# Kernel tuning notes

Measured on AMD Instinct MI355X. Metric: run time of the kernel, lower is better.

The kernel has to match this reference:

```python
import jax, jax.numpy as jnp
import numpy as np

B, S, DIM = 2, 2048, 2048
H, DN, DR, DV, L = 16, 128, 64, 128, 512  # heads, nope, rope, v, kv_lora_rank
EPS = 1e-5


def setup_inputs() -> dict:
    key = jax.random.key(0)
    ks = jax.random.split(key, 12)
    x = jax.random.normal(ks[0], (B, S, DIM), dtype=jnp.float32)
    # rotary tables (DeepSeek-style: theta = 10000^{-2i/d})
    inv_freq = 1.0 / (10000.0 ** (jnp.arange(0, DR, 2, dtype=jnp.float32) / DR))
    ang = jnp.arange(S, dtype=jnp.float32)[:, None] * inv_freq[None, :]  # [S, DR/2]
    freqs_cos = jnp.cos(ang)
    freqs_sin = jnp.sin(ang)
    w = 0.02
    wq_w = jax.random.normal(ks[1], (H * (DN + DR), DIM), dtype=jnp.float32) * w
    wq_b = jnp.zeros((H * (DN + DR),), dtype=jnp.float32)
    wkv_a_w = jax.random.normal(ks[2], (L + DR, DIM), dtype=jnp.float32) * w
    wkv_a_b = jnp.zeros((L + DR,), dtype=jnp.float32)
    kv_norm_g = jnp.ones((L,), dtype=jnp.float32)
    kv_norm_b = jnp.zeros((L,), dtype=jnp.float32)
    wkv_b_w = jax.random.normal(ks[3], (H * (DN + DV), L), dtype=jnp.float32) * w
    wo_w = jax.random.normal(ks[4], (DIM, H * DV), dtype=jnp.float32) * w
    wo_b = jnp.zeros((DIM,), dtype=jnp.float32)
    return {"x": x, "start_pos": 0, "freqs_cos": freqs_cos, "freqs_sin": freqs_sin,
            "wq_w": wq_w, "wq_b": wq_b, "wkv_a_w": wkv_a_w, "wkv_a_b": wkv_a_b,
            "kv_norm_g": kv_norm_g, "kv_norm_b": kv_norm_b, "wkv_b_w": wkv_b_w,
            "wo_w": wo_w, "wo_b": wo_b}


def _rope(t, cos, sin):
    # t: [B, S, n, DR] interpreted as interleaved (re, im) pairs
    tr = t.reshape(*t.shape[:-1], DR // 2, 2)
    re, im = tr[..., 0], tr[..., 1]
    c = cos[None, :, None, :]
    s = sin[None, :, None, :]
    out = jnp.stack([re * c - im * s, re * s + im * c], axis=-1)
    return out.reshape(t.shape)


def _layernorm(v, g, b):
    mu = jnp.mean(v, axis=-1, keepdims=True)
    var = jnp.mean(jnp.square(v - mu), axis=-1, keepdims=True)
    return (v - mu) * jax.lax.rsqrt(var + EPS) * g + b


def reference(x, start_pos, freqs_cos, freqs_sin, wq_w, wq_b, wkv_a_w, wkv_a_b,
              kv_norm_g, kv_norm_b, wkv_b_w, wo_w, wo_b):
    bsz, seqlen, _ = x.shape
    scale = (DN + DR) ** -0.5
    # q projection
    q = (x @ wq_w.T + wq_b).reshape(bsz, seqlen, H, DN + DR)
    q_nope, q_pe = q[..., :DN], q[..., DN:]
    q_pe = _rope(q_pe, freqs_cos, freqs_sin)
    # kv projection
    kv_full = x @ wkv_a_w.T + wkv_a_b
    kv, k_pe = kv_full[..., :L], kv_full[..., L:]
    k_pe = _rope(k_pe[:, :, None, :], freqs_cos, freqs_sin)[:, :, 0, :]  # [B,S,DR]
    kvn = _layernorm(kv, kv_norm_g, kv_norm_b)  # compressed kv cache entries [B,S,L]
    wkv_b = wkv_b_w.reshape(H, DN + DV, L)
    # absorption: fold wkv_b's k-part into q_nope
    q_abs = jnp.einsum('bshd,hdc->bshc', q_nope, wkv_b[:, :DN])
    scores = (jnp.einsum('bshc,btc->bsht', q_abs, kvn)
              + jnp.einsum('bshr,btr->bsht', q_pe, k_pe)) * scale
    # causal mask (query global pos = start_pos + s, key pos = t)
    qpos = jnp.arange(seqlen) + start_pos
    tpos = jnp.arange(seqlen)
    causal = qpos[:, None] >= tpos[None, :]  # [S, T]
    scores = jnp.where(causal[None, :, None, :], scores, -jnp.inf)
    p = jax.nn.softmax(scores.astype(jnp.float32), axis=-1).astype(x.dtype)
    # compressed attention output then un-absorb v
    ctx = jnp.einsum('bsht,btc->bshc', p, kvn)
    out = jnp.einsum('bshc,hdc->bshd', ctx, wkv_b[:, -DV:])
    return out.reshape(bsz, seqlen, H * DV) @ wo_w.T + wo_b
```

## Files before the change

kernel.cpp:

```cpp
#include <hip/hip_runtime.h>
#include <stdint.h>

typedef __attribute__((ext_vector_type(8))) __bf16 bf16x8;
typedef __attribute__((ext_vector_type(4))) float  f32x4;
typedef __attribute__((ext_vector_type(8))) unsigned short u16x8;
typedef __attribute__((ext_vector_type(2))) unsigned int u32x2;
typedef __attribute__((ext_vector_type(4))) unsigned int u32x4;

typedef __attribute__((address_space(1))) void AS1void;
typedef __attribute__((address_space(3))) void AS3void;
typedef __attribute__((address_space(3))) const unsigned char AS3c;

__device__ __forceinline__ float b2f(unsigned short u) {
  unsigned x = ((unsigned)u) << 16; float f; __builtin_memcpy(&f, &x, 4); return f;
}
__device__ __forceinline__ unsigned short f2b(float f) {
  unsigned x; __builtin_memcpy(&x, &f, 4);
  unsigned r = (x + 0x7fffu + ((x >> 16) & 1u)) >> 16;
  return (unsigned short)r;
}
__device__ __forceinline__ void gload16(const void* g, void* l) {
  __builtin_amdgcn_global_load_lds((AS1void*)(void*)g, (AS3void*)l, 16, 0, 0);
}
__device__ __forceinline__ bf16x8 mk8(u32x2 a, u32x2 b) {
  u32x4 t; t[0] = a[0]; t[1] = a[1]; t[2] = b[0]; t[3] = b[1];
  bf16x8 r; __builtin_memcpy(&r, &t, 16); return r;
}
template<int OFF>
__device__ __forceinline__ u32x2 tr_read(AS3c* vp) {
  u32x2 r;
  asm volatile("ds_read_b64_tr_b16 %0, %1 offset:%2"
               : "=&v"(r) : "v"(vp), "n"(OFF));
  return r;
}

__global__ __launch_bounds__(256) void k_cast(const float* __restrict__ in,
                                              unsigned short* __restrict__ out, long n) {
  long i = ((long)blockIdx.x * 256 + threadIdx.x) * 4;
  if (i >= n) return;
  float4 v = *(const float4*)(in + i);
  ushort4 o;
  o.x = f2b(v.x); o.y = f2b(v.y); o.z = f2b(v.z); o.w = f2b(v.w);
  *(ushort4*)(out + i) = o;
}

__global__ __launch_bounds__(256) void k_prep_wkvb(const float* __restrict__ wkvb,
                                                   unsigned short* __restrict__ kT,
                                                   unsigned short* __restrict__ vv) {
  long i = (long)blockIdx.x * 256 + threadIdx.x;
  {
    int d = (int)(i & 127); long r = i >> 7; int c = (int)(r & 511); int h = (int)(r >> 9);
    kT[i] = f2b(wkvb[((long)(h * 256 + d)) * 512 + c]);
  }
  {
    int c = (int)(i & 511); long r = i >> 9; int d = (int)(r & 127); int h = (int)(r >> 7);
    vv[i] = f2b(wkvb[((long)(h * 256 + 128 + d)) * 512 + c]);
  }
}

template<int OUTF32, int BIAS>
__global__ __launch_bounds__(256, 2) void k_gemm_bt(
    const unsigned short* __restrict__ A, long lda, long aSb, long aSh,
    const unsigned short* __restrict__ B, long ldb, long bSb, long bSh,
    void* __restrict__ Cp, long ldc, long cSb, long cSh,
    const float* __restrict__ bias,
    int M, int N, int K, int zH) {
  __shared__ __align__(16) unsigned short sA[128 * 32];
  __shared__ __align__(16) unsigned short sB[128 * 32];
  const int z = blockIdx.z, zb = z / zH, zh = z % zH;
  const unsigned short* Ab = A + zb * aSb + zh * aSh;
  const unsigned short* Bb = B + zb * bSb + zh * bSh;
  const long cOff = (long)zb * cSb + (long)zh * cSh;
  const int n0 = blockIdx.x * 128, m0 = blockIdx.y * 128;
  const int t = threadIdx.x, w = t >> 6, l = t & 63;
  const int wr = (w >> 1) * 64, wc = (w & 1) * 64;
  const int lr = l & 15, lg = l >> 4;
  f32x4 acc[4][4] = {};
  for (int k0 = 0; k0 < K; k0 += 32) {
    #pragma unroll
    for (int cc = 0; cc < 2; ++cc) {
      int c = t + cc * 256;
      int row = c >> 2, col = (c & 3) * 8;
      int ar = m0 + row; ar = ar < M ? ar : M - 1;
      int br = n0 + row; br = br < N ? br : N - 1;
      gload16(Ab + (long)ar * lda + k0 + col, (char*)sA + c * 16);
      gload16(Bb + (long)br * ldb + k0 + col, (char*)sB + c * 16);
    }
    __syncthreads();
    bf16x8 af[4], bf[4];
    #pragma unroll
    for (int i = 0; i < 4; ++i) af[i] = *(const bf16x8*)&sA[(wr + i * 16 + lr) * 32 + lg * 8];
    #pragma unroll
    for (int j = 0; j < 4; ++j) bf[j] = *(const bf16x8*)&sB[(wc + j * 16 + lr) * 32 + lg * 8];
    #pragma unroll
    for (int i = 0; i < 4; ++i)
      #pragma unroll
      for (int j = 0; j < 4; ++j)
        acc[i][j] = __builtin_amdgcn_mfma_f32_16x16x32_bf16(af[i], bf[j], acc[i][j], 0, 0, 0);
    __syncthreads();
  }
  #pragma unroll
  for (int i = 0; i < 4; ++i) {
    #pragma unroll
    for (int r = 0; r < 4; ++r) {
      int row = m0 + wr + i * 16 + lg * 4 + r;
      if (row >= M) continue;
      #pragma unroll
      for (int j = 0; j < 4; ++j) {
        int col = n0 + wc + j * 16 + lr;
        if (col >= N) continue;
        float v = acc[i][j][r];
        if (BIAS) v += bias[col];
        if (OUTF32) ((float*)Cp)[cOff + (long)row * ldc + col] = v;
        else ((unsigned short*)Cp)[cOff + (long)row * ldc + col] = f2b(v);
      }
    }
  }
}

__global__ __launch_bounds__(256) void k_ln(const unsigned short* __restrict__ kvb,
                                            const float* __restrict__ g,
                                            const float* __restrict__ be,
                                            unsigned short* __restrict__ kcat) {
  const int w = threadIdx.x >> 6, l = threadIdx.x & 63;
  const long row = (long)blockIdx.x * 4 + w;
  const unsigned short* src = kvb + row * 576 + l * 8;
  u16x8 v = *(const u16x8*)src;
  float f[8]; float s = 0.f, s2 = 0.f;
  #pragma unroll
  for (int j = 0; j < 8; ++j) { f[j] = b2f(v[j]); s += f[j]; s2 += f[j] * f[j]; }
  #pragma unroll
  for (int m = 1; m < 64; m <<= 1) { s += __shfl_xor(s, m); s2 += __shfl_xor(s2, m); }
  float mu = s * (1.f / 512.f);
  float var = s2 * (1.f / 512.f) - mu * mu;
  float rs = rsqrtf(var + 1e-5f);
  u16x8 o;
  #pragma unroll
  for (int j = 0; j < 8; ++j) {
    int c = l * 8 + j;
    o[j] = f2b((f[j] - mu) * rs * g[c] + be[c]);
  }
  *(u16x8*)(kcat + row * 576 + l * 8) = o;
}

__global__ __launch_bounds__(256) void k_rope_k(const unsigned short* __restrict__ kvb,
                                                const float* __restrict__ fc,
                                                const float* __restrict__ fs,
                                                unsigned short* __restrict__ kcat) {
  int i = blockIdx.x * 256 + threadIdx.x;
  int p = i & 31; int r = i >> 5;
  int s = r & 2047; int b = r >> 11;
  long base = ((long)(b * 2048 + s)) * 576 + 512 + 2 * p;
  float re = b2f(kvb[base]), im = b2f(kvb[base + 1]);
  float c = fc[s * 32 + p], sn = fs[s * 32 + p];
  kcat[base] = f2b(re * c - im * sn);
  kcat[base + 1] = f2b(re * sn + im * c);
}

__global__ __launch_bounds__(256) void k_rope_q(const unsigned short* __restrict__ qfull,
                                                const float* __restrict__ fc,
                                                const float* __restrict__ fs,
                                                unsigned short* __restrict__ qcat) {
  long i = (long)blockIdx.x * 256 + threadIdx.x;
  int p = (int)(i & 31); long r = i >> 5;
  int h = (int)(r & 15); r >>= 4;
  int s = (int)(r & 2047); int b = (int)(r >> 11);
  const unsigned short* src = qfull + ((long)(b * 2048 + s)) * 3072 + h * 192 + 128 + 2 * p;
  float re = b2f(src[0]), im = b2f(src[1]);
  float c = fc[s * 32 + p], sn = fs[s * 32 + p];
  unsigned short* dst = qcat + ((long)((b * 16 + h) * 2048 + s)) * 576 + 512 + 2 * p;
  dst[0] = f2b(re * c - im * sn);
  dst[1] = f2b(re * sn + im * c);
}

__global__ __launch_bounds__(256, 2) void k_attn(
    const unsigned short* __restrict__ qcat,
    const unsigned short* __restrict__ kcat,
    unsigned short* __restrict__ ctx,
    const int* __restrict__ spp) {
  __shared__ __align__(16) char smem[78336];
  const int id = blockIdx.x;
  const int rr = id & 7;
  const int b = rr >> 2;
  const int local = (id >> 3) * 4 + (rr & 3);
  const int qb = 31 - (local >> 4);
  const int h = local & 15;
  const int t = threadIdx.x, w = t >> 6, l = t & 63;
  const int lq = l & 15, hh = l >> 4;
  const int sp = spp[0];
  const long bh = (long)(b * 16 + h);
  const long qrow0 = bh * 2048 + qb * 64 + w * 16;
  const float scale = 0.07216878364870323f;

  bf16x8 qf[18];
  #pragma unroll
  for (int kk = 0; kk < 18; ++kk)
    qf[kk] = *(const bf16x8*)&qcat[(qrow0 + lq) * 576 + kk * 32 + hh * 8];

  f32x4 acc[8][4];
  #pragma unroll
  for (int i = 0; i < 8; ++i)
    #pragma unroll
    for (int j = 0; j < 4; ++j) acc[i][j] = (f32x4){0.f, 0.f, 0.f, 0.f};
  float mrun = -1e30f, lrun = 0.f;
  const int qg = qb * 64 + w * 16 + lq + sp;
  int tmax = qb * 64 + 63 + sp; if (tmax > 2047) tmax = 2047;

  const unsigned short* kbase = kcat + (long)b * 2048 * 576;

  auto STAGE = [&](int bi, int t0) {
    char* dK = smem + bi * 36864;
    #pragma unroll
    for (int cc = 0; cc < 9; ++cc) {
      int c = t + cc * 256;
      int tt = ((c >> 3) & 7) * 4 + ((c >> 1) & 3);
      int gc = (c >> 6) * 16 + (c & 1) * 8;
      gload16(kbase + (long)(t0 + tt) * 576 + gc, dK + c * 16);
    }
  };

  STAGE(0, 0);
  int cur = 0;
  unsigned short* sP = (unsigned short*)(smem + 73728);
  float* sAl = (float*)(smem + 77824);
  int* sNeed = (int*)(smem + 78080);
  const int qrow = w * 16 + lq;
  const int xq = ((qrow >> 1) & 3) << 4;
  const int vcol = (hh * 16) ^ (((lq >> 1) & 3) << 4);
  const int kq = ((lq >> 2) << 7) + ((lq & 3) << 5) + ((hh & 1) << 4) + ((hh >> 1) << 10);

  for (int t0 = 0; t0 <= tmax; t0 += 32) {
    const bool pref = (t0 + 32 <= tmax);
    if (pref) {
      STAGE(cur ^ 1, t0 + 32);
      asm volatile("s_waitcnt vmcnt(9)" ::: "memory");
    } else {
      asm volatile("s_waitcnt vmcnt(0)" ::: "memory");
    }
    __builtin_amdgcn_sched_barrier(0);
    __builtin_amdgcn_s_barrier();
    __builtin_amdgcn_sched_barrier(0);

    const char* sKc = smem + cur * 36864;
    f32x4 sc[2];
    sc[0] = (f32x4){0.f,0.f,0.f,0.f}; sc[1] = (f32x4){0.f,0.f,0.f,0.f};
    __builtin_amdgcn_s_setprio(1);
    #pragma unroll
    for (int tf = 0; tf < 2; ++tf) {
      const char* rb = sKc + kq + tf * 512;
      #pragma unroll
      for (int kk = 0; kk < 18; ++kk) {
        bf16x8 kf = *(const bf16x8*)(rb + kk * 2048);
        sc[tf] = __builtin_amdgcn_mfma_f32_16x16x32_bf16(kf, qf[kk], sc[tf], 0, 0, 0);
      }
    }
    __builtin_amdgcn_s_setprio(0);

    float v[2][4];
    float mt = -1e30f;
    #pragma unroll
    for (int tf = 0; tf < 2; ++tf)
      #pragma unroll
      for (int r = 0; r < 4; ++r) {
        int tg = t0 + tf * 16 + 4 * hh + r;
        v[tf][r] = (tg <= qg) ? sc[tf][r] * scale : -1e30f;
        mt = fmaxf(mt, v[tf][r]);
      }
    mt = fmaxf(mt, __shfl_xor(mt, 16));
    mt = fmaxf(mt, __shfl_xor(mt, 32));
    float al = 1.f;
    unsigned long long needb = __ballot(mt > mrun + 8.f);
    if (needb) {
      float mn = fmaxf(mrun, mt);
      al = __expf(mrun - mn);
      mrun = mn;
      lrun *= al;
    }
    float sr = 0.f;
    #pragma unroll
    for (int tf = 0; tf < 2; ++tf) {
      ushort4 pk;
      float e0 = __expf(v[tf][0] - mrun);
      float e1 = __expf(v[tf][1] - mrun);
      float e2 = __expf(v[tf][2] - mrun);
      float e3 = __expf(v[tf][3] - mrun);
      sr += (e0 + e1) + (e2 + e3);
      pk.x = f2b(e0); pk.y = f2b(e1); pk.z = f2b(e2); pk.w = f2b(e3);
      *(ushort4*)((char*)sP + qrow * 64 + ((32 * tf + 8 * hh) ^ xq)) = pk;
    }
    sr += __shfl_xor(sr, 16);
    sr += __shfl_xor(sr, 32);
    lrun += sr;
    if (l < 16) sAl[w * 16 + l] = al;
    if (l == 0) sNeed[w] = needb ? 1 : 0;
    asm volatile("s_waitcnt lgkmcnt(0)" ::: "memory");
    __builtin_amdgcn_sched_barrier(0);
    __builtin_amdgcn_s_barrier();
    __builtin_amdgcn_sched_barrier(0);

    int needAny = sNeed[0] | sNeed[1] | sNeed[2] | sNeed[3];
    if (needAny) {
      float a4[4];
      #pragma unroll
      for (int q2 = 0; q2 < 4; ++q2) a4[q2] = sAl[q2 * 16 + lq];
      #pragma unroll
      for (int cb = 0; cb < 8; ++cb)
        #pragma unroll
        for (int q2 = 0; q2 < 4; ++q2) acc[cb][q2] *= a4[q2];
    }
    bf16x8 pf0 = *(const bf16x8*)((char*)sP + (0 * 16 + lq) * 64 + vcol);
    bf16x8 pf1 = *(const bf16x8*)((char*)sP + (1 * 16 + lq) * 64 + vcol);
    bf16x8 pf2 = *(const bf16x8*)((char*)sP + (2 * 16 + lq) * 64 + vcol);
    bf16x8 pf3 = *(const bf16x8*)((char*)sP + (3 * 16 + lq) * 64 + vcol);
    __builtin_amdgcn_sched_barrier(0);
    AS3c* vp3 = (AS3c*)(smem + cur * 36864 + (w * 8192) + hh * 256 + lq * 8);
    u32x2 A0, A1, B0, B1, C0, C1, D0, D1;
    #define TRR2(d0, d1, CB) do { \
      d0 = tr_read<(CB) * 1024>(vp3); \
      d1 = tr_read<(CB) * 1024 + 128>(vp3); } while (0)
    #define PVC(CB, E0, E1) do { \
      bf16x8 vf = mk8(E0, E1); \
      acc[CB][0] = __builtin_amdgcn_mfma_f32_16x16x32_bf16(vf, pf0, acc[CB][0], 0, 0, 0); \
      acc[CB][1] = __builtin_amdgcn_mfma_f32_16x16x32_bf16(vf, pf1, acc[CB][1], 0, 0, 0); \
      acc[CB][2] = __builtin_amdgcn_mfma_f32_16x16x32_bf16(vf, pf2, acc[CB][2], 0, 0, 0); \
      acc[CB][3] = __builtin_amdgcn_mfma_f32_16x16x32_bf16(vf, pf3, acc[CB][3], 0, 0, 0); } while (0)
    TRR2(A0, A1, 0); TRR2(B0, B1, 1);
    TRR2(C0, C1, 2); TRR2(D0, D1, 3);
    asm volatile("s_waitcnt lgkmcnt(4)" ::: "memory");
    __builtin_amdgcn_sched_barrier(0);
    __builtin_amdgcn_s_setprio(1);
    PVC(0, A0, A1); PVC(1, B0, B1);
    __builtin_amdgcn_s_setprio(0);
    TRR2(A0, A1, 4); TRR2(B0, B1, 5);
    asm volatile("s_waitcnt lgkmcnt(4)" ::: "memory");
    __builtin_amdgcn_sched_barrier(0);
    __builtin_amdgcn_s_setprio(1);
    PVC(2, C0, C1); PVC(3, D0, D1);
    __builtin_amdgcn_s_setprio(0);
    TRR2(C0, C1, 6); TRR2(D0, D1, 7);
    asm volatile("s_waitcnt lgkmcnt(4)" ::: "memory");
    __builtin_amdgcn_sched_barrier(0);
    __builtin_amdgcn_s_setprio(1);
    PVC(4, A0, A1); PVC(5, B0, B1);
    __builtin_amdgcn_s_setprio(0);
    asm volatile("s_waitcnt lgkmcnt(0)" ::: "memory");
    __builtin_amdgcn_sched_barrier(0);
    __builtin_amdgcn_s_setprio(1);
    PVC(6, C0, C1); PVC(7, D0, D1);
    __builtin_amdgcn_s_setprio(0);
    #undef TRR2
    #undef PVC
    __builtin_amdgcn_sched_barrier(0);
    __builtin_amdgcn_s_barrier();
    __builtin_amdgcn_sched_barrier(0);
    cur ^= 1;
  }

  if (l < 16) sAl[w * 16 + l] = lrun;
  __syncthreads();
  float linv[4];
  #pragma unroll
  for (int q2 = 0; q2 < 4; ++q2) linv[q2] = 1.0f / sAl[q2 * 16 + lq];
  unsigned short* eb = (unsigned short*)smem;
  #pragma unroll
  for (int cb = 0; cb < 8; ++cb) {
    const int c0 = w * 128 + cb * 16 + hh * 4;
    #pragma unroll
    for (int q2 = 0; q2 < 4; ++q2) {
      f32x4 a = acc[cb][q2];
      ushort4 o;
      o.x = f2b(a[0] * linv[q2]); o.y = f2b(a[1] * linv[q2]);
      o.z = f2b(a[2] * linv[q2]); o.w = f2b(a[3] * linv[q2]);
      *(ushort4*)&eb[(q2 * 16 + lq) * 528 + c0] = o;
    }
  }
  __syncthreads();
  unsigned short* Co = ctx + (bh * 2048 + qb * 64) * 512;
  #pragma unroll
  for (int i = 0; i < 16; ++i) {
    int id2 = t + i * 256;
    int row = id2 >> 6, col = (id2 & 63) * 8;
    *(u16x8*)&Co[(long)row * 512 + col] = *(const u16x8*)&eb[row * 528 + col];
  }
}

extern "C" void kernel_launch(void* const* d_in, const int* in_sizes, int n_in,
                              void* d_out, int out_size, void* d_ws, size_t ws_size,
                              hipStream_t stream) {
  const float* x      = (const float*)d_in[0];
  const int*   sp     = (const int*)d_in[1];
  const float* fcos   = (const float*)d_in[2];
  const float* fsin   = (const float*)d_in[3];
  const float* wq_w   = (const float*)d_in[4];
  const float* wq_b   = (const float*)d_in[5];
  const float* wkva_w = (const float*)d_in[6];
  const float* wkva_b = (const float*)d_in[7];
  const float* lng    = (const float*)d_in[8];
  const float* lnb    = (const float*)d_in[9];
  const float* wkvb_w = (const float*)d_in[10];
  const float* wo_w   = (const float*)d_in[11];
  const float* wo_b   = (const float*)d_in[12];
  float* out = (float*)d_out;

  if (ws_size < 171180032) return;

  char* ws = (char*)d_ws;
  unsigned short* xb     = (unsigned short*)(ws + 0);
  unsigned short* wqbf   = (unsigned short*)(ws + 16777216);
  unsigned short* qfull  = (unsigned short*)(ws + 29360128);
  unsigned short* ctx    = (unsigned short*)(ws + 0);
  unsigned short* wkvabf = (unsigned short*)(ws + 67108864);
  unsigned short* wkvbkT = (unsigned short*)(ws + 69468160);
  unsigned short* wkvbv  = (unsigned short*)(ws + 71565312);
  unsigned short* wobf   = (unsigned short*)(ws + 73662464);
  unsigned short* kvbf   = (unsigned short*)(ws + 82051072);
  unsigned short* kcat   = (unsigned short*)(ws + 86769664);
  unsigned short* qcat   = (unsigned short*)(ws + 95682560);
  unsigned short* outh   = qcat;

  k_cast<<<8192, 256, 0, stream>>>(x, xb, 8388608L);
  k_cast<<<6144, 256, 0, stream>>>(wq_w, wqbf, 6291456L);
  k_cast<<<1152, 256, 0, stream>>>(wkva_w, wkvabf, 1179648L);
  k_cast<<<4096, 256, 0, stream>>>(wo_w, wobf, 4194304L);
  k_prep_wkvb<<<4096, 256, 0, stream>>>(wkvb_w, wkvbkT, wkvbv);

  k_gemm_bt<0, 1><<<dim3(24, 32, 1), 256, 0, stream>>>(
      xb, 2048, 0, 0, wqbf, 2048, 0, 0, qfull, 3072, 0, 0, wq_b, 4096, 3072, 2048, 1);
  k_gemm_bt<0, 1><<<dim3(5, 32, 1), 256, 0, stream>>>(
      xb, 2048, 0, 0, wkvabf, 2048, 0, 0, kvbf, 576, 0, 0, wkva_b, 4096, 576, 2048, 1);

  k_ln<<<1024, 256, 0, stream>>>(kvbf, lng, lnb, kcat);
  k_rope_k<<<512, 256, 0, stream>>>(kvbf, fcos, fsin, kcat);
  k_rope_q<<<16384, 256, 0, stream>>>(qfull, fcos, fsin, qcat);

  k_gemm_bt<0, 0><<<dim3(4, 16, 32), 256, 0, stream>>>(
      qfull, 3072, (long)2048 * 3072, 192,
      wkvbkT, 128, 0, (long)512 * 128,
      qcat, 576, (long)16 * 2048 * 576, (long)2048 * 576,
      nullptr, 2048, 512, 128, 16);

  k_attn<<<dim3(1024, 1, 1), 256, 0, stream>>>(qcat, kcat, ctx, sp);

  k_gemm_bt<0, 0><<<dim3(1, 16, 32), 256, 0, stream>>>(
      ctx, 512, (long)16 * 2048 * 512, (long)2048 * 512,
      wkvbv, 512, 0, (long)128 * 512,
      outh, 2048, (long)2048 * 2048, 128,
      nullptr, 2048, 128, 512, 16);

  k_gemm_bt<1, 1><<<dim3(16, 32, 1), 256, 0, stream>>>(
      outh, 2048, 0, 0, wobf, 2048, 0, 0, out, 2048, 0, 0, wo_b, 4096, 2048, 2048, 1);
}
```

Measured before the change: 623.4 us.

## Single-buffer attention K tile to cut LDS and raise GEMM occupancy hint

The attention kernel drops its double-buffered K/V staging for a single LDS buffer, roughly halving shared memory. It now loads each tile and waits for it before computing, so global-load prefetch no longer overlaps compute. The epilogue is split into two half passes so the smaller LDS can still hold the output staging. Separately, the GEMM launch bound is raised to 4 blocks per CU, which may force register limits or spills in exchange for more resident waves.

```diff
diff --git a/kernel.cpp b/kernel.cpp
--- a/kernel.cpp
+++ b/kernel.cpp
@@ -59,7 +59,7 @@
 }
 
 template<int OUTF32, int BIAS>
-__global__ __launch_bounds__(256, 2) void k_gemm_bt(
+__global__ __launch_bounds__(256, 4) void k_gemm_bt(
     const unsigned short* __restrict__ A, long lda, long aSb, long aSh,
     const unsigned short* __restrict__ B, long ldb, long bSb, long bSh,
     void* __restrict__ Cp, long ldc, long cSb, long cSh,
@@ -178,7 +178,7 @@
     const unsigned short* __restrict__ kcat,
     unsigned short* __restrict__ ctx,
     const int* __restrict__ spp) {
-  __shared__ __align__(16) char smem[78336];
+  __shared__ __align__(16) char smem[41248];
   const int id = blockIdx.x;
   const int rr = id & 7;
   const int b = rr >> 2;
@@ -208,46 +208,33 @@
 
   const unsigned short* kbase = kcat + (long)b * 2048 * 576;
 
-  auto STAGE = [&](int bi, int t0) {
-    char* dK = smem + bi * 36864;
+  unsigned short* sP = (unsigned short*)(smem + 36864);
+  float* sAl = (float*)(smem + 40960);
+  int* sNeed = (int*)(smem + 41216);
+  const int qrow = w * 16 + lq;
+  const int xq = ((qrow >> 1) & 3) << 4;
+  const int vcol = (hh * 16) ^ (((lq >> 1) & 3) << 4);
+  const int kq = ((lq >> 2) << 7) + ((lq & 3) << 5) + ((hh & 1) << 4) + ((hh >> 1) << 10);
+
+  for (int t0 = 0; t0 <= tmax; t0 += 32) {
     #pragma unroll
     for (int cc = 0; cc < 9; ++cc) {
       int c = t + cc * 256;
       int tt = ((c >> 3) & 7) * 4 + ((c >> 1) & 3);
       int gc = (c >> 6) * 16 + (c & 1) * 8;
-      gload16(kbase + (long)(t0 + tt) * 576 + gc, dK + c * 16);
-    }
-  };
-
-  STAGE(0, 0);
-  int cur = 0;
-  unsigned short* sP = (unsigned short*)(smem + 73728);
-  float* sAl = (float*)(smem + 77824);
-  int* sNeed = (int*)(smem + 78080);
-  const int qrow = w * 16 + lq;
-  const int xq = ((qrow >> 1) & 3) << 4;
-  const int vcol = (hh * 16) ^ (((lq >> 1) & 3) << 4);
-  const int kq = ((lq >> 2) << 7) + ((lq & 3) << 5) + ((hh & 1) << 4) + ((hh >> 1) << 10);
-
-  for (int t0 = 0; t0 <= tmax; t0 += 32) {
-    const bool pref = (t0 + 32 <= tmax);
-    if (pref) {
-      STAGE(cur ^ 1, t0 + 32);
-      asm volatile("s_waitcnt vmcnt(9)" ::: "memory");
-    } else {
-      asm volatile("s_waitcnt vmcnt(0)" ::: "memory");
-    }
+      gload16(kbase + (long)(t0 + tt) * 576 + gc, smem + c * 16);
+    }
+    asm volatile("s_waitcnt vmcnt(0)" ::: "memory");
     __builtin_amdgcn_sched_barrier(0);
     __builtin_amdgcn_s_barrier();
     __builtin_amdgcn_sched_barrier(0);
 
-    const char* sKc = smem + cur * 36864;
     f32x4 sc[2];
     sc[0] = (f32x4){0.f,0.f,0.f,0.f}; sc[1] = (f32x4){0.f,0.f,0.f,0.f};
     __builtin_amdgcn_s_setprio(1);
     #pragma unroll
     for (int tf = 0; tf < 2; ++tf) {
-      const char* rb = sKc + kq + tf * 512;
+      const char* rb = smem + kq + tf * 512;
       #pragma unroll
       for (int kk = 0; kk < 18; ++kk) {
         bf16x8 kf = *(const bf16x8*)(rb + kk * 2048);
@@ -313,7 +300,7 @@
     bf16x8 pf2 = *(const bf16x8*)((char*)sP + (2 * 16 + lq) * 64 + vcol);
     bf16x8 pf3 = *(const bf16x8*)((char*)sP + (3 * 16 + lq) * 64 + vcol);
     __builtin_amdgcn_sched_barrier(0);
-    AS3c* vp3 = (AS3c*)(smem + cur * 36864 + (w * 8192) + hh * 256 + lq * 8);
+    AS3c* vp3 = (AS3c*)(smem + (w * 8192) + hh * 256 + lq * 8);
     u32x2 A0, A1, B0, B1, C0, C1, D0, D1;
     #define TRR2(d0, d1, CB) do { \
       d0 = tr_read<(CB) * 1024>(vp3); \
@@ -353,7 +340,6 @@
     __builtin_amdgcn_sched_barrier(0);
     __builtin_amdgcn_s_barrier();
     __builtin_amdgcn_sched_barrier(0);
-    cur ^= 1;
   }
 
   if (l < 16) sAl[w * 16 + l] = lrun;
@@ -362,25 +348,30 @@
   #pragma unroll
   for (int q2 = 0; q2 < 4; ++q2) linv[q2] = 1.0f / sAl[q2 * 16 + lq];
   unsigned short* eb = (unsigned short*)smem;
-  #pragma unroll
-  for (int cb = 0; cb < 8; ++cb) {
-    const int c0 = w * 128 + cb * 16 + hh * 4;
-    #pragma unroll
-    for (int q2 = 0; q2 < 4; ++q2) {
-      f32x4 a = acc[cb][q2];
-      ushort4 o;
-      o.x = f2b(a[0] * linv[q2]); o.y = f2b(a[1] * linv[q2]);
-      o.z = f2b(a[2] * linv[q2]); o.w = f2b(a[3] * linv[q2]);
-      *(ushort4*)&eb[(q2 * 16 + lq) * 528 + c0] = o;
-    }
-  }
-  __syncthreads();
   unsigned short* Co = ctx + (bh * 2048 + qb * 64) * 512;
   #pragma unroll
-  for (int i = 0; i < 16; ++i) {
-    int id2 = t + i * 256;
-    int row = id2 >> 6, col = (id2 & 63) * 8;
-    *(u16x8*)&Co[(long)row * 512 + col] = *(const u16x8*)&eb[row * 528 + col];
+  for (int p = 0; p < 2; ++p) {
+    __syncthreads();
+    #pragma unroll
+    for (int cb = 0; cb < 8; ++cb) {
+      const int c0 = w * 128 + cb * 16 + hh * 4;
+      #pragma unroll
+      for (int q2 = 0; q2 < 2; ++q2) {
+        int qq = p * 2 + q2;
+        f32x4 a = acc[cb][qq];
+        ushort4 o;
+        o.x = f2b(a[0] * linv[qq]); o.y = f2b(a[1] * linv[qq]);
+        o.z = f2b(a[2] * linv[qq]); o.w = f2b(a[3] * linv[qq]);
+        *(ushort4*)&eb[(q2 * 16 + lq) * 528 + c0] = o;
+      }
+    }
+    __syncthreads();
+    #pragma unroll
+    for (int i = 0; i < 8; ++i) {
+      int id2 = t + i * 256;
+      int row = id2 >> 6, col = (id2 & 63) * 8;
+      *(u16x8*)&Co[(long)(p * 32 + row) * 512 + col] = *(const u16x8*)&eb[row * 528 + col];
+    }
   }
 }
 
```

After: 635.3 us. About the same (+1.9%).
